# Kernel tuning notes

Hardware: AMD Instinct MI355X
Metric: run time of the kernel (lower is better)

The kernel has to match this reference:

```python
import jax, jax.numpy as jnp
import numpy as np

KD = 128; N_STU_TAB = 20000; N_EXER_TAB = 20000
NS = 4096; NE = 4096; NK = 128
E_SE = 131072; E_EK = 16384; B = 8192
ALPHAS = 0.1; ALPHAE = 0.1; TAU = 0.5


def setup_inputs():
    key = jax.random.key(0)
    ks = jax.random.split(key, 32)
    f = lambda i, shape, s=0.09: jax.random.normal(ks[i], shape, dtype=jnp.float32) * s
    ri = lambda i, shape, hi: jax.random.randint(ks[i], shape, 0, hi)
    inp = {
        'E_stu': f(0, (N_STU_TAB, KD), 0.1),
        'E_exer': f(1, (N_EXER_TAB, KD), 0.1),
        'E_k': f(2, (NK, KD), 0.1),
        'W1': f(3, (KD, KD)), 'a1s': f(4, (KD,)), 'a1d': f(5, (KD,)),
        'W2': f(6, (KD, KD)), 'a2s': f(7, (KD,)), 'a2d': f(8, (KD,)),
        'pW1': f(9, (KD, KD)), 'pW2': f(10, (KD, KD)),
        'pW3': f(11, (KD, KD)), 'pb3': jnp.zeros((KD,), jnp.float32),
        'kn_r': (jax.random.uniform(ks[12], (B, KD)) < 0.25).astype(jnp.float32) + 1e-3,
        'stu_ids': ri(13, (NS,), N_STU_TAB),
        'exer_ids': ri(14, (NE,), N_EXER_TAB),
        'k_ids': jnp.arange(NK),
    }
    j = 15
    for g in ('g0', 'g1', 'g2'):
        inp['se_src_' + g] = ri(j, (E_SE,), NS); j += 1
        inp['se_dst_' + g] = ri(j, (E_SE,), NE); j += 1
        inp['ek_src_' + g] = ri(j, (E_EK,), NE); j += 1
        inp['ek_dst_' + g] = ri(j, (E_EK,), NK); j += 1
    inp['stu_index'] = ri(j, (B,), NS); j += 1
    inp['exer_index'] = ri(j, (B,), NE)
    return inp


def _seg_softmax_agg(scores, msgs, dst, n):
    # numerically-stable softmax over edges grouped by destination node
    m = jax.ops.segment_max(scores, dst, num_segments=n)
    m = jnp.where(jnp.isfinite(m), m, 0.0)
    ex = jnp.exp(scores - m[dst])
    den = jax.ops.segment_sum(ex, dst, num_segments=n)
    alpha = ex / (den[dst] + 1e-16)
    return jax.ops.segment_sum(alpha[:, None] * msgs, dst, num_segments=n)


def _gat(emb, edges, W, a_s, a_d):
    # single-head GAT over hetero edges: stu<->exer, exer<->k
    hs, he, hk = emb['stu'] @ W, emb['exer'] @ W, emb['k'] @ W
    ss_s, ss_e, ss_k = hs @ a_s, he @ a_s, hk @ a_s   # src attention terms
    sd_s, sd_e, sd_k = hs @ a_d, he @ a_d, hk @ a_d   # dst attention terms
    se_src, se_dst, ek_src, ek_dst = edges
    lrelu = lambda x: jax.nn.leaky_relu(x, 0.2)
    # stu <- exer (reverse of stu->exer edges)
    sc = lrelu(ss_e[se_dst] + sd_s[se_src])
    new_s = jax.nn.elu(_seg_softmax_agg(sc, he[se_dst], se_src, NS))
    # exer <- stu  and  exer <- k (softmax spans both relations)
    sc1 = lrelu(ss_s[se_src] + sd_e[se_dst])
    sc2 = lrelu(ss_k[ek_dst] + sd_e[ek_src])
    sc = jnp.concatenate([sc1, sc2])
    msg = jnp.concatenate([hs[se_src], hk[ek_dst]])
    dst = jnp.concatenate([se_dst, ek_src])
    new_e = jax.nn.elu(_seg_softmax_agg(sc, msg, dst, NE))
    # k <- exer
    sc = lrelu(ss_e[ek_src] + sd_k[ek_dst])
    new_k = jax.nn.elu(_seg_softmax_agg(sc, he[ek_src], ek_dst, NK))
    return {'stu': new_s, 'exer': new_e, 'k': new_k}


def _closs(h1, h2):
    z1 = h1 / (jnp.linalg.norm(h1, axis=1, keepdims=True) + 1e-12)
    z2 = h2 / (jnp.linalg.norm(h2, axis=1, keepdims=True) + 1e-12)
    sim = z1 @ z2.T                      # [N, N] cosine similarity
    ex = jnp.exp(sim / TAU)
    pos = jnp.diagonal(ex)
    neg = ex.sum(axis=1) - pos           # off-diagonal sum
    return jnp.mean(-jnp.log(pos / (pos + neg)))


def reference(E_stu, E_exer, E_k, W1, a1s, a1d, W2, a2s, a2d,
              pW1, pW2, pW3, pb3, kn_r,
              stu_ids, exer_ids, k_ids,
              se_src_g0, se_dst_g0, ek_src_g0, ek_dst_g0,
              se_src_g1, se_dst_g1, ek_src_g1, ek_dst_g1,
              se_src_g2, se_dst_g2, ek_src_g2, ek_dst_g2,
              stu_index, exer_index):
    e0 = {'stu': E_stu[stu_ids], 'exer': E_exer[exer_ids], 'k': E_k[k_ids]}

    def run(edges):
        e1 = _gat(e0, edges, W1, a1s, a1d)
        return _gat(e1, edges, W2, a2s, a2d)

    main = run((se_src_g0, se_dst_g0, ek_src_g0, ek_dst_g0))
    v1 = run((se_src_g1, se_dst_g1, ek_src_g1, ek_dst_g1))
    v2 = run((se_src_g2, se_dst_g2, ek_src_g2, ek_dst_g2))

    closs = (ALPHAS * (_closs(v1['stu'], v2['stu']) + _closs(v2['stu'], v1['stu']))
             + ALPHAE * (_closs(v1['exer'], v2['exer']) + _closs(v2['exer'], v1['exer'])))

    bs = main['stu'][stu_index]          # [B, KD]
    be = main['exer'][exer_index]        # [B, KD]
    pref = jax.nn.sigmoid(bs @ pW1.T)
    diff = jax.nn.sigmoid(be @ pW2.T)
    o = jax.nn.sigmoid((pref - diff) @ pW3.T + pb3)
    out = (o * kn_r).sum(axis=1) / kn_r.sum(axis=1)
    return out[:, None], closs
```

## Files before the change

kernel.cpp:

```cpp
#include <hip/hip_runtime.h>
#include <hip/hip_bf16.h>
#include <math.h>

#define KD 128
#define NS 4096
#define NE 4096
#define NK 128
#define NNODE (NS + NE + NK)
#define ESE 131072
#define EEK 16384
#define NCSR (2*ESE + 2*EEK)
#define BQ 8192
#define RP (NNODE + 1)
#define HB 32

typedef __attribute__((ext_vector_type(8))) short short8;
typedef __attribute__((ext_vector_type(4))) short short4_;
typedef __attribute__((ext_vector_type(4))) float float4_;

__device__ __forceinline__ float lrelu_(float x){ return x >= 0.f ? x : 0.2f*x; }
__device__ __forceinline__ float elu_(float x){ return x > 0.f ? x : __expf(x) - 1.f; }
__device__ __forceinline__ float sigm_(float x){ return 1.f/(1.f + __expf(-x)); }
__device__ __forceinline__ float bf2f_(unsigned short u){
  union { unsigned int i; float f; } v; v.i = ((unsigned int)u) << 16; return v.f;
}
__device__ __forceinline__ unsigned short f2b_(float x){
  __hip_bfloat16 b = __float2bfloat16(x); return *(unsigned short*)&b;
}

struct EdgePtrs { const int* s_src[3]; const int* s_dst[3]; const int* e_src[3]; const int* e_dst[3]; };

__global__ __launch_bounds__(256)
void k_fuse1(EdgePtrs ep, int* __restrict__ part,
             const float* __restrict__ W1, const float* __restrict__ a1s,
             const float* __restrict__ a1d,
             unsigned short* __restrict__ hb0, float* __restrict__ ss0,
             float* __restrict__ sd0,
             const float* __restrict__ E_stu, const float* __restrict__ E_exer,
             const float* __restrict__ E_k, const int* __restrict__ sid,
             const int* __restrict__ eid, const int* __restrict__ kid,
             const float* __restrict__ pW1, const float* __restrict__ pW2,
             const float* __restrict__ pW3, unsigned short* __restrict__ pWb,
             const float* __restrict__ W2, unsigned short* __restrict__ w2b) {
  __shared__ __align__(16) char smem[NNODE*4];
  int bid = blockIdx.x, t = threadIdx.x;

  if (bid < 3*HB) {
    int* hcnt = (int*)smem;
    int g = bid / HB, b = bid % HB;
    for (int i = t; i < NNODE; i += 256) hcnt[i] = 0;
    __syncthreads();
    const int* ss_ = ep.s_src[g]; const int* sd_ = ep.s_dst[g];
    const int* es_ = ep.e_src[g]; const int* ed_ = ep.e_dst[g];
    int se0 = b*(ESE/HB);
    for (int i = se0 + t; i < se0 + ESE/HB; i += 256) {
      atomicAdd(&hcnt[ss_[i]], 1);
      atomicAdd(&hcnt[NS + sd_[i]], 1);
    }
    int ek0 = b*(EEK/HB);
    for (int i = ek0 + t; i < ek0 + EEK/HB; i += 256) {
      atomicAdd(&hcnt[NS + es_[i]], 1);
      atomicAdd(&hcnt[NS + NE + ed_[i]], 1);
    }
    __syncthreads();
    int* pp = part + ((size_t)g*HB + b)*NNODE;
    for (int i = t; i < NNODE; i += 256) pp[i] = hcnt[i];
    return;
  }

  if (bid < 3*HB + NNODE/32) {
    float (*ers)[KD] = (float(*)[KD])smem;
    int row0 = (bid - 3*HB)*32;
    int w = t >> 6, c = t & 63;
    for (int i = t; i < 32*KD; i += 256) {
      int r = i >> 7, k = i & 127;
      int gr = row0 + r;
      const float* srow;
      if (gr < NS)           srow = E_stu  + (size_t)sid[gr]*KD;
      else if (gr < NS + NE) srow = E_exer + (size_t)eid[gr - NS]*KD;
      else                   srow = E_k    + (size_t)kid[gr - NS - NE]*KD;
      ers[r][k] = srow[k];
    }
    __syncthreads();
    float acc0[8] = {0,0,0,0,0,0,0,0}, acc1[8] = {0,0,0,0,0,0,0,0};
    #pragma unroll 2
    for (int kc = 0; kc < KD; kc += 4) {
      float wa[4], wb[4];
      #pragma unroll
      for (int j = 0; j < 4; j++) {
        wa[j] = W1[(kc + j)*KD + c];
        wb[j] = W1[(kc + j)*KD + c + 64];
      }
      #pragma unroll
      for (int r = 0; r < 8; r++) {
        float4 e = *(const float4*)&ers[w*8 + r][kc];
        acc0[r] += e.x*wa[0] + e.y*wa[1] + e.z*wa[2] + e.w*wa[3];
        acc1[r] += e.x*wb[0] + e.y*wb[1] + e.z*wb[2] + e.w*wb[3];
      }
    }
    float as1 = a1s[c], as2 = a1s[c + 64], ad1 = a1d[c], ad2 = a1d[c + 64];
    #pragma unroll
    for (int r = 0; r < 8; r++) {
      int gr = row0 + w*8 + r;
      hb0[(size_t)gr*KD + c]      = f2b_(acc0[r]);
      hb0[(size_t)gr*KD + c + 64] = f2b_(acc1[r]);
      float s = acc0[r]*as1 + acc1[r]*as2;
      float d = acc0[r]*ad1 + acc1[r]*ad2;
      #pragma unroll
      for (int off = 32; off; off >>= 1) { s += __shfl_xor(s, off); d += __shfl_xor(d, off); }
      if (c == 0) { ss0[gr] = s; sd0[gr] = d; }
    }
    return;
  }

  {
    int idx = bid - 3*HB - NNODE/32;
    if (idx < 16) {
      float (*tile)[33] = (float(*)[33])smem;
      int tx = t & 31, ty = t >> 5;
      int bx = (idx & 3)*32, by = (idx >> 2)*32;
      for (int j = 0; j < 32; j += 8)
        tile[ty + j][tx] = W2[(by + ty + j)*KD + bx + tx];
      __syncthreads();
      for (int j = 0; j < 32; j += 8)
        w2b[(bx + ty + j)*KD + by + tx] = f2b_(tile[tx][ty + j]);
    } else {
      int r = idx - 16;
      const float* src = r < 4 ? pW1 : (r < 8 ? pW2 : pW3);
      unsigned short* dst = pWb + (size_t)(r >> 2)*KD*KD;
      int off = (r & 3)*4096;
      for (int i = t; i < 1024; i += 256) {
        float4 v = *(const float4*)&src[off + i*4];
        short4_ s;
        s[0] = (short)f2b_(v.x); s[1] = (short)f2b_(v.y);
        s[2] = (short)f2b_(v.z); s[3] = (short)f2b_(v.w);
        *(short4_*)&dst[off + i*4] = s;
      }
    }
  }
}

__global__ void k_sumpart(const int* __restrict__ part, int* __restrict__ cnt_all) {
  int idx = blockIdx.x*256 + threadIdx.x;
  if (idx >= 3*NNODE) return;
  int g = idx / NNODE, n = idx - g*NNODE;
  const int* pg = part + (size_t)g*HB*NNODE + n;
  int s = 0;
  #pragma unroll
  for (int b = 0; b < HB; b++) s += pg[(size_t)b*NNODE];
  cnt_all[idx] = s;
}

__global__ void k_scan(const int* __restrict__ cnt_all, int* __restrict__ rp_all) {
  __shared__ int sums[1024];
  const int CH = (NNODE + 1023) / 1024;
  int g = blockIdx.x, t = threadIdx.x;
  const int* cnt = cnt_all + g*NNODE;
  int* row_ptr = rp_all + g*RP;
  int base = t*CH;
  int local[CH];
  int s = 0;
  for (int j = 0; j < CH; j++) {
    int v = (base + j < NNODE) ? cnt[base + j] : 0;
    local[j] = s; s += v;
  }
  sums[t] = s; __syncthreads();
  for (int off = 1; off < 1024; off <<= 1) {
    int v = (t >= off) ? sums[t - off] : 0;
    __syncthreads();
    sums[t] += v;
    __syncthreads();
  }
  int excl = (t == 0) ? 0 : sums[t - 1];
  for (int j = 0; j < CH; j++)
    if (base + j < NNODE) row_ptr[base + j] = excl + local[j];
  if (t == 1023) row_ptr[NNODE] = sums[1023];
}

__global__ void k_boff(const int* __restrict__ part, const int* __restrict__ rp_all,
                       int* __restrict__ boff) {
  int idx = blockIdx.x*256 + threadIdx.x;
  if (idx >= 3*NNODE) return;
  int g = idx / NNODE, n = idx - g*NNODE;
  const int* pg = part + (size_t)g*HB*NNODE + n;
  int* bg = boff + (size_t)g*HB*NNODE + n;
  int acc = rp_all[g*RP + n];
  #pragma unroll
  for (int b = 0; b < HB; b++) {
    bg[(size_t)b*NNODE] = acc;
    acc += pg[(size_t)b*NNODE];
  }
}

__global__ __launch_bounds__(256)
void k_scatter(EdgePtrs ep, const int* __restrict__ boff, unsigned short* __restrict__ col_all) {
  __shared__ int cur[NNODE];
  int g = blockIdx.y, b = blockIdx.x, t = threadIdx.x;
  const int* bg = boff + ((size_t)g*HB + b)*NNODE;
  for (int i = t; i < NNODE; i += 256) cur[i] = bg[i];
  __syncthreads();
  const int* ss_ = ep.s_src[g]; const int* sd_ = ep.s_dst[g];
  const int* es_ = ep.e_src[g]; const int* ed_ = ep.e_dst[g];
  unsigned short* col = col_all + (size_t)g*NCSR;
  int se0 = b*(ESE/HB);
  for (int i = se0 + t; i < se0 + ESE/HB; i += 256) {
    int s = ss_[i], d = NS + sd_[i];
    col[atomicAdd(&cur[s], 1)] = (unsigned short)d;
    col[atomicAdd(&cur[d], 1)] = (unsigned short)s;
  }
  int ek0 = b*(EEK/HB);
  for (int i = ek0 + t; i < ek0 + EEK/HB; i += 256) {
    int s = NS + es_[i], d = NS + NE + ed_[i];
    col[atomicAdd(&cur[s], 1)] = (unsigned short)d;
    col[atomicAdd(&cur[d], 1)] = (unsigned short)s;
  }
}

__global__ __launch_bounds__(256)
void k_mgemm(const unsigned short* __restrict__ X, const unsigned short* __restrict__ WT,
             const float* __restrict__ a_s, const float* __restrict__ a_d,
             unsigned short* __restrict__ hb, float* __restrict__ ss,
             float* __restrict__ sd) {
  __shared__ unsigned short As[128*KD];
  __shared__ unsigned short Bs[128*KD];
  __shared__ float ssp[128][2], sdp[128][2];
  int t = threadIdx.x;
  const unsigned short* Arow = X + (size_t)blockIdx.x*128*KD;
  #pragma unroll
  for (int j = 0; j < 8; j++) {
    int G = t + j*256;
    int r = G >> 4, g = G & 15;
    int sw = g ^ (r & 15);
    *(float4*)&As[(r*16 + sw)*8] = *(const float4*)&Arow[(size_t)G*8];
    *(float4*)&Bs[(r*16 + sw)*8] = *(const float4*)&WT[(size_t)G*8];
  }
  __syncthreads();
  int w = t >> 6, lane = t & 63;
  int rw = (w >> 1)*64, cw = (w & 1)*64;
  int m15 = lane & 15, quad = lane >> 4;
  float4_ acc[4][4] = {};
  #pragma unroll
  for (int kq = 0; kq < 4; kq++) {
    short8 a[4], b[4];
    int g = kq*4 + quad;
    #pragma unroll
    for (int mi = 0; mi < 4; mi++) {
      int r = rw + mi*16 + m15;
      a[mi] = *(const short8*)&As[(r*16 + (g ^ (r & 15)))*8];
    }
    #pragma unroll
    for (int ni = 0; ni < 4; ni++) {
      int r = cw + ni*16 + m15;
      b[ni] = *(const short8*)&Bs[(r*16 + (g ^ (r & 15)))*8];
    }
    #pragma unroll
    for (int mi = 0; mi < 4; mi++)
      #pragma unroll
      for (int ni = 0; ni < 4; ni++)
        acc[mi][ni] = __builtin_amdgcn_mfma_f32_16x16x32_bf16(a[mi], b[ni], acc[mi][ni], 0, 0, 0);
  }
  int row0 = blockIdx.x*128;
  float asv[4], adv[4];
  #pragma unroll
  for (int ni = 0; ni < 4; ni++) {
    int gc = cw + ni*16 + m15;
    asv[ni] = a_s[gc]; adv[ni] = a_d[gc];
  }
  #pragma unroll
  for (int mi = 0; mi < 4; mi++) {
    #pragma unroll
    for (int reg = 0; reg < 4; reg++) {
      int lr = rw + mi*16 + quad*4 + reg;
      int gr = row0 + lr;
      float s = 0.f, d = 0.f;
      #pragma unroll
      for (int ni = 0; ni < 4; ni++) {
        float v = acc[mi][ni][reg];
        hb[(size_t)gr*KD + cw + ni*16 + m15] = f2b_(v);
        s += v*asv[ni]; d += v*adv[ni];
      }
      s += __shfl_xor(s, 1); d += __shfl_xor(d, 1);
      s += __shfl_xor(s, 2); d += __shfl_xor(d, 2);
      s += __shfl_xor(s, 4); d += __shfl_xor(d, 4);
      s += __shfl_xor(s, 8); d += __shfl_xor(d, 8);
      if (m15 == 0) { ssp[lr][w & 1] = s; sdp[lr][w & 1] = d; }
    }
  }
  __syncthreads();
  if (t < 128) {
    ss[row0 + t] = ssp[t][0] + ssp[t][1];
    sd[row0 + t] = sdp[t][0] + sdp[t][1];
  }
}

__global__ __launch_bounds__(256)
void k_headm(const unsigned short* __restrict__ pWb,
             const float* __restrict__ pb, const float* __restrict__ knr,
             float* __restrict__ out, const float* __restrict__ pbuf,
             const float* __restrict__ g1,
             const int* __restrict__ i1, const int* __restrict__ i2) {
  __shared__ unsigned short At[32*KD];
  __shared__ unsigned short Bt[32*KD];
  __shared__ unsigned short Xt[32*KD];
  __shared__ float nump[32][2], denp[32][2];
  int t = threadIdx.x;
  int row0 = blockIdx.x*32;
  for (int i = t; i < 512; i += 256) {
    int r = i >> 4, g = i & 15;
    int sw = g ^ (r & 15);
    {
      const float* src = &g1[(size_t)i1[row0 + r]*KD + g*8];
      float4 v0 = *(const float4*)src, v1 = *(const float4*)(src + 4);
      short8 s;
      s[0] = (short)f2b_(v0.x); s[1] = (short)f2b_(v0.y);
      s[2] = (short)f2b_(v0.z); s[3] = (short)f2b_(v0.w);
      s[4] = (short)f2b_(v1.x); s[5] = (short)f2b_(v1.y);
      s[6] = (short)f2b_(v1.z); s[7] = (short)f2b_(v1.w);
      *(short8*)&At[(r*16 + sw)*8] = s;
    }
    {
      const float* src = &g1[(size_t)(NS + i2[row0 + r])*KD + g*8];
      float4 v0 = *(const float4*)src, v1 = *(const float4*)(src + 4);
      short8 s;
      s[0] = (short)f2b_(v0.x); s[1] = (short)f2b_(v0.y);
      s[2] = (short)f2b_(v0.z); s[3] = (short)f2b_(v0.w);
      s[4] = (short)f2b_(v1.x); s[5] = (short)f2b_(v1.y);
      s[6] = (short)f2b_(v1.z); s[7] = (short)f2b_(v1.w);
      *(short8*)&Bt[(r*16 + sw)*8] = s;
    }
  }
  __syncthreads();
  int w = t >> 6, lane = t & 63;
  int rw = (w >> 1)*16, cw = (w & 1)*64;
  int m15 = lane & 15, quad = lane >> 4;
  const unsigned short* W1g = pWb;
  const unsigned short* W2g = pWb + KD*KD;
  const unsigned short* W3g = pWb + 2*KD*KD;
  float4_ accP[4] = {}, accD[4] = {};
  #pragma unroll
  for (int kq = 0; kq < 4; kq++) {
    int g = kq*4 + quad;
    int ra = rw + m15;
    short8 a1 = *(const short8*)&At[(ra*16 + (g ^ (ra & 15)))*8];
    short8 a2 = *(const short8*)&Bt[(ra*16 + (g ^ (ra & 15)))*8];
    #pragma unroll
    for (int ni = 0; ni < 4; ni++) {
      int rb = cw + ni*16 + m15;
      short8 b1 = *(const short8*)&W1g[(size_t)rb*KD + g*8];
      short8 b2 = *(const short8*)&W2g[(size_t)rb*KD + g*8];
      accP[ni] = __builtin_amdgcn_mfma_f32_16x16x32_bf16(a1, b1, accP[ni], 0, 0, 0);
      accD[ni] = __builtin_amdgcn_mfma_f32_16x16x32_bf16(a2, b2, accD[ni], 0, 0, 0);
    }
  }
  #pragma unroll
  for (int ni = 0; ni < 4; ni++) {
    #pragma unroll
    for (int reg = 0; reg < 4; reg++) {
      int lr = rw + quad*4 + reg;
      int col = cw + ni*16 + m15;
      float diff = sigm_(accP[ni][reg]) - sigm_(accD[ni][reg]);
      int g2 = col >> 3;
      Xt[(lr*16 + (g2 ^ (lr & 15)))*8 + (col & 7)] = f2b_(diff);
    }
  }
  __syncthreads();
  float4_ accO[4] = {};
  #pragma unroll
  for (int kq = 0; kq < 4; kq++) {
    int g = kq*4 + quad;
    int ra = rw + m15;
    short8 a = *(const short8*)&Xt[(ra*16 + (g ^ (ra & 15)))*8];
    #pragma unroll
    for (int ni = 0; ni < 4; ni++) {
      int rb = cw + ni*16 + m15;
      short8 b = *(const short8*)&W3g[(size_t)rb*KD + g*8];
      accO[ni] = __builtin_amdgcn_mfma_f32_16x16x32_bf16(a, b, accO[ni], 0, 0, 0);
    }
  }
  float pbv[4];
  #pragma unroll
  for (int ni = 0; ni < 4; ni++) pbv[ni] = pb[cw + ni*16 + m15];
  #pragma unroll
  for (int reg = 0; reg < 4; reg++) {
    int lr = rw + quad*4 + reg;
    int gr = row0 + lr;
    float num = 0.f, den = 0.f;
    #pragma unroll
    for (int ni = 0; ni < 4; ni++) {
      float kr = knr[(size_t)gr*KD + cw + ni*16 + m15];
      float o = sigm_(accO[ni][reg] + pbv[ni]);
      num += o*kr; den += kr;
    }
    num += __shfl_xor(num, 1); den += __shfl_xor(den, 1);
    num += __shfl_xor(num, 2); den += __shfl_xor(den, 2);
    num += __shfl_xor(num, 4); den += __shfl_xor(den, 4);
    num += __shfl_xor(num, 8); den += __shfl_xor(den, 8);
    if (m15 == 0) { nump[lr][w & 1] = num; denp[lr][w & 1] = den; }
  }
  __syncthreads();
  if (t < 32)
    out[row0 + t] = (nump[t][0] + nump[t][1]) / (denp[t][0] + denp[t][1]);
  if (blockIdx.x == 0 && w == 0) {
    float v = (lane < 32) ? pbuf[lane] : 0.f;
    #pragma unroll
    for (int off = 32; off; off >>= 1) v += __shfl_xor(v, off);
    if (lane == 0) out[BQ] = 0.1f*v/(float)NS;
  }
}

__global__ __launch_bounds__(256)
void k_agg(const int* __restrict__ rp_all, const unsigned short* __restrict__ col_all,
           const unsigned short* __restrict__ hb_base, const float* __restrict__ ss,
           const float* __restrict__ sd, unsigned short* __restrict__ outb,
           float* __restrict__ out, unsigned short* __restrict__ Zo, int gsel) {
  int wv = blockIdx.x*4 + (threadIdx.x >> 6);
  int lane = threadIdx.x & 63;
  if (wv >= 3*NNODE) return;
  int g = wv / NNODE, node = wv - g*NNODE;
  bool layer2 = (gsel == -2);
  if (layer2 && node >= NS + NE) return;
  const int* rp = rp_all + g*RP;
  const unsigned short* cl = col_all + (size_t)g*NCSR;
  const unsigned short* hgb = layer2 ? hb_base + (size_t)g*NNODE*KD : hb_base;
  const float* ssg = layer2 ? ss + g*NNODE : ss;
  const float* sdg = layer2 ? sd + g*NNODE : sd;
  int e0 = rp[node], e1 = rp[node + 1];
  float sdv = sdg[node];
  int sub = lane >> 4;
  int fl  = lane & 15;
  float l = 0.f;
  float A[8] = {0,0,0,0,0,0,0,0};
  #pragma unroll 4
  for (int e = e0 + sub; e < e1; e += 4) {
    int o = cl[e];
    float pj = __expf(lrelu_(ssg[o] + sdv));
    l += pj;
    short8 mv = *(const short8*)&hgb[(size_t)o*KD + fl*8];
    #pragma unroll
    for (int q = 0; q < 8; q++)
      A[q] += pj * bf2f_((unsigned short)mv[q]);
  }
  l += __shfl_xor(l, 16); l += __shfl_xor(l, 32);
  #pragma unroll
  for (int q = 0; q < 8; q++) {
    A[q] += __shfl_xor(A[q], 16);
    A[q] += __shfl_xor(A[q], 32);
  }
  float inv = 1.f/(l + 1e-16f);
  float av[8];
  #pragma unroll
  for (int q = 0; q < 8; q++) av[q] = elu_(A[q]*inv);
  if (!layer2) {
    if (sub == 0) {
      short8 sv;
      #pragma unroll
      for (int q = 0; q < 8; q++) sv[q] = (short)f2b_(av[q]);
      *(short8*)&outb[(size_t)wv*KD + fl*8] = sv;
    }
    return;
  }
  if (g == 0) {
    if (sub == 0) {
      float* orow = &out[(size_t)node*KD + fl*8];
      *(float4*)orow       = make_float4(av[0], av[1], av[2], av[3]);
      *(float4*)(orow + 4) = make_float4(av[4], av[5], av[6], av[7]);
    }
  } else {
    float nrm = av[0]*av[0] + av[1]*av[1] + av[2]*av[2] + av[3]*av[3]
              + av[4]*av[4] + av[5]*av[5] + av[6]*av[6] + av[7]*av[7];
    #pragma unroll
    for (int off = 1; off <= 8; off <<= 1) nrm += __shfl_xor(nrm, off);
    float invn = 1.f/(sqrtf(nrm) + 1e-12f);
    if (sub == 0) {
      short8 sv;
      #pragma unroll
      for (int q = 0; q < 8; q++) sv[q] = (short)f2b_(av[q]*invn);
      *(short8*)&Zo[((size_t)(g - 1)*8192 + node)*KD + fl*8] = sv;
    }
  }
}

__global__ __launch_bounds__(256)
void k_sim(const unsigned short* __restrict__ Z, float* __restrict__ rsp,
           float* __restrict__ csp, float* __restrict__ dg_all) {
  __shared__ unsigned short As[128*KD];
  __shared__ unsigned short Bs[128*KD];
  int z = blockIdx.z;
  int t = threadIdx.x;
  const unsigned short* Arow = Z + ((size_t)z*NS + (size_t)blockIdx.x*128)*KD;
  const unsigned short* Brow = Z + ((size_t)8192 + (size_t)z*NS + (size_t)blockIdx.y*128)*KD;
  #pragma unroll
  for (int j = 0; j < 8; j++) {
    int G = t + j*256;
    int r = G >> 4, g = G & 15;
    int sw = g ^ (r & 15);
    *(float4*)&As[(r*16 + sw)*8] = *(const float4*)&Arow[(size_t)G*8];
    *(float4*)&Bs[(r*16 + sw)*8] = *(const float4*)&Brow[(size_t)G*8];
  }
  __syncthreads();
  int w = t >> 6, lane = t & 63;
  int rw = (w >> 1)*64, cw = (w & 1)*64;
  int m15 = lane & 15, quad = lane >> 4;
  float4_ acc[4][4] = {};
  #pragma unroll
  for (int kq = 0; kq < 4; kq++) {
    short8 a[4], b[4];
    int g = kq*4 + quad;
    #pragma unroll
    for (int mi = 0; mi < 4; mi++) {
      int r = rw + mi*16 + m15;
      a[mi] = *(const short8*)&As[(r*16 + (g ^ (r & 15)))*8];
    }
    #pragma unroll
    for (int ni = 0; ni < 4; ni++) {
      int r = cw + ni*16 + m15;
      b[ni] = *(const short8*)&Bs[(r*16 + (g ^ (r & 15)))*8];
    }
    #pragma unroll
    for (int mi = 0; mi < 4; mi++)
      #pragma unroll
      for (int ni = 0; ni < 4; ni++)
        acc[mi][ni] = __builtin_amdgcn_mfma_f32_16x16x32_bf16(a[mi], b[ni], acc[mi][ni], 0, 0, 0);
  }
  int i0 = blockIdx.x*128, j0 = blockIdx.y*128;
  float* diag = dg_all + z*NS;
  float* rrow = rsp + ((size_t)z*64 + blockIdx.y*2 + (w & 1))*NS;
  float* crow = csp + ((size_t)z*64 + blockIdx.x*2 + (w >> 1))*NS;
  float cs[4] = {0,0,0,0};
  #pragma unroll
  for (int mi = 0; mi < 4; mi++) {
    float rs[4] = {0,0,0,0};
    #pragma unroll
    for (int ni = 0; ni < 4; ni++) {
      #pragma unroll
      for (int reg = 0; reg < 4; reg++) {
        float sim2 = acc[mi][ni][reg]*2.0f;
        int gi = i0 + rw + mi*16 + quad*4 + reg;
        int gj = j0 + cw + ni*16 + m15;
        if (gi == gj) diag[gi] = sim2;
        float e = __expf(sim2);
        rs[reg] += e; cs[ni] += e;
      }
    }
    #pragma unroll
    for (int reg = 0; reg < 4; reg++) {
      float v = rs[reg];
      v += __shfl_xor(v, 1); v += __shfl_xor(v, 2);
      v += __shfl_xor(v, 4); v += __shfl_xor(v, 8);
      if (m15 == 0) rrow[i0 + rw + mi*16 + quad*4 + reg] = v;
    }
  }
  #pragma unroll
  for (int ni = 0; ni < 4; ni++) {
    float v = cs[ni];
    v += __shfl_xor(v, 16); v += __shfl_xor(v, 32);
    if (quad == 0) crow[j0 + cw + ni*16 + m15] = v;
  }
}

__global__ void k_lred(const float* __restrict__ rsp, const float* __restrict__ csp,
                       const float* __restrict__ dg_all, float* __restrict__ pbuf) {
  __shared__ float red[256];
  int z = blockIdx.y;
  int i = blockIdx.x*256 + threadIdx.x;
  float rs = 0.f, cs = 0.f;
  for (int s = 0; s < 64; s++) {
    rs += rsp[((size_t)z*64 + s)*NS + i];
    cs += csp[((size_t)z*64 + s)*NS + i];
  }
  float v = logf(rs) + logf(cs) - 2.f*dg_all[z*NS + i];
  red[threadIdx.x] = v; __syncthreads();
  for (int off = 128; off; off >>= 1) {
    if (threadIdx.x < off) red[threadIdx.x] += red[threadIdx.x + off];
    __syncthreads();
  }
  if (threadIdx.x == 0) pbuf[z*16 + blockIdx.x] = red[0];
}

extern "C" void kernel_launch(void* const* d_in, const int* in_sizes, int n_in,
                              void* d_out, int out_size, void* d_ws, size_t ws_size,
                              hipStream_t stream) {
  const float* E_stu  = (const float*)d_in[0];
  const float* E_exer = (const float*)d_in[1];
  const float* E_k    = (const float*)d_in[2];
  const float* W1  = (const float*)d_in[3];
  const float* a1s = (const float*)d_in[4];
  const float* a1d = (const float*)d_in[5];
  const float* W2  = (const float*)d_in[6];
  const float* a2s = (const float*)d_in[7];
  const float* a2d = (const float*)d_in[8];
  const float* pW1 = (const float*)d_in[9];
  const float* pW2 = (const float*)d_in[10];
  const float* pW3 = (const float*)d_in[11];
  const float* pb3 = (const float*)d_in[12];
  const float* kn_r = (const float*)d_in[13];
  const int* stu_ids  = (const int*)d_in[14];
  const int* exer_ids = (const int*)d_in[15];
  const int* k_ids    = (const int*)d_in[16];
  EdgePtrs ep;
  for (int g = 0; g < 3; g++) {
    ep.s_src[g] = (const int*)d_in[17 + g*4];
    ep.s_dst[g] = (const int*)d_in[18 + g*4];
    ep.e_src[g] = (const int*)d_in[19 + g*4];
    ep.e_dst[g] = (const int*)d_in[20 + g*4];
  }
  const int* stu_index  = (const int*)d_in[29];
  const int* exer_index = (const int*)d_in[30];
  float* out = (float*)d_out;

  char* p = (char*)d_ws;
  auto carve = [&](size_t bytes) -> char* {
    char* r = p; p += (bytes + 255) & ~(size_t)255; return r;
  };
  const size_t NODE_F = (size_t)NNODE*KD;
  float* ssb = (float*)carve((size_t)8*NNODE*4);
  float* ss0 = ssb,            *sd0 = ssb + NNODE;
  float* ss3 = ssb + 2*NNODE,  *sd3 = ssb + 5*NNODE;
  unsigned short* hb0 = (unsigned short*)carve(NODE_F*2);
  unsigned short* hb3 = (unsigned short*)carve(3*NODE_F*2);
  char* Creg = carve((size_t)8*HB*NNODE*4);
  int*   part = (int*)Creg;
  int*   boff = (int*)Creg + (size_t)3*HB*NNODE;
  unsigned short* etb = (unsigned short*)Creg;
  float* eoutAll = (float*)carve((size_t)(NS + NE)*KD*4);
  int* cnt_all = (int*)carve((size_t)3*NNODE*4);
  int* rp_all  = (int*)carve((size_t)3*RP*4);
  unsigned short* col_all = (unsigned short*)carve((size_t)3*NCSR*2);
  unsigned short* pWb = (unsigned short*)carve((size_t)3*KD*KD*2);
  float* rsp = (float*)carve((size_t)2*64*NS*4);
  float* csp = (float*)carve((size_t)2*64*NS*4);
  float* dg_all = (float*)carve((size_t)2*NS*4);
  float* pbuf = (float*)carve(64*4);
  unsigned short* Z = (unsigned short*)carve((size_t)2*8192*KD*2);
  unsigned short* w2b = (unsigned short*)carve((size_t)KD*KD*2);

  k_fuse1<<<3*HB + NNODE/32 + 16 + 12, 256, 0, stream>>>(
      ep, part, W1, a1s, a1d, hb0, ss0, sd0,
      E_stu, E_exer, E_k, stu_ids, exer_ids, k_ids,
      pW1, pW2, pW3, pWb, W2, w2b);

  k_sumpart<<<(3*NNODE + 255)/256, 256, 0, stream>>>(part, cnt_all);
  k_scan<<<3, 1024, 0, stream>>>(cnt_all, rp_all);
  k_boff<<<(3*NNODE + 255)/256, 256, 0, stream>>>(part, rp_all, boff);
  k_scatter<<<dim3(HB, 3), 256, 0, stream>>>(ep, boff, col_all);

  k_agg<<<3*NNODE/4, 256, 0, stream>>>(rp_all, col_all, hb0, ss0, sd0, etb,
                                       nullptr, nullptr, -1);

  k_mgemm<<<3*NNODE/128, 256, 0, stream>>>(etb, w2b, a2s, a2d, hb3, ss3, sd3);
  k_agg<<<3*NNODE/4, 256, 0, stream>>>(rp_all, col_all, hb3, ss3, sd3, nullptr,
                                       eoutAll, Z, -2);

  k_sim<<<dim3(32, 32, 2), 256, 0, stream>>>(Z, rsp, csp, dg_all);
  k_lred<<<dim3(16, 2), 256, 0, stream>>>(rsp, csp, dg_all, pbuf);

  k_headm<<<BQ/32, 256, 0, stream>>>(pWb, pb3, kn_r,
                                     out, pbuf, eoutAll, stu_index, exer_index);
}
```

Measured before the change: 275.2 us.

## Fuse prediction head into similarity kernel and finalize loss via atomics

Merges the prediction-head kernel into the contrastive-similarity kernel as extra blocks of one launch, so the two independent workloads share the GPU and one launch is removed. The main-view aggregation output is now stored as bf16 rather than fp32, which halves that write and lets the head load it without converting. The final loss reduction moves into k_lred through an atomic accumulator and a last-block counter, with the accumulator reset in k_boff. In exchange it adds atomics and a threadfence-based completion pattern, and the fused kernel's shared-memory footprint is sized for the similarity path.

New measurement: 270.1 us. About the same (-1.8%).

```diff
diff --git a/kernel.cpp b/kernel.cpp
--- a/kernel.cpp
+++ b/kernel.cpp
@@ -178,8 +178,9 @@
 }
 
 __global__ void k_boff(const int* __restrict__ part, const int* __restrict__ rp_all,
-                       int* __restrict__ boff) {
+                       int* __restrict__ boff, float* __restrict__ clbuf) {
   int idx = blockIdx.x*256 + threadIdx.x;
+  if (idx == 0) { clbuf[0] = 0.f; ((int*)clbuf)[1] = 0; }
   if (idx >= 3*NNODE) return;
   int g = idx / NNODE, n = idx - g*NNODE;
   const int* pg = part + (size_t)g*HB*NNODE + n;
@@ -294,125 +295,10 @@
 }
 
 __global__ __launch_bounds__(256)
-void k_headm(const unsigned short* __restrict__ pWb,
-             const float* __restrict__ pb, const float* __restrict__ knr,
-             float* __restrict__ out, const float* __restrict__ pbuf,
-             const float* __restrict__ g1,
-             const int* __restrict__ i1, const int* __restrict__ i2) {
-  __shared__ unsigned short At[32*KD];
-  __shared__ unsigned short Bt[32*KD];
-  __shared__ unsigned short Xt[32*KD];
-  __shared__ float nump[32][2], denp[32][2];
-  int t = threadIdx.x;
-  int row0 = blockIdx.x*32;
-  for (int i = t; i < 512; i += 256) {
-    int r = i >> 4, g = i & 15;
-    int sw = g ^ (r & 15);
-    {
-      const float* src = &g1[(size_t)i1[row0 + r]*KD + g*8];
-      float4 v0 = *(const float4*)src, v1 = *(const float4*)(src + 4);
-      short8 s;
-      s[0] = (short)f2b_(v0.x); s[1] = (short)f2b_(v0.y);
-      s[2] = (short)f2b_(v0.z); s[3] = (short)f2b_(v0.w);
-      s[4] = (short)f2b_(v1.x); s[5] = (short)f2b_(v1.y);
-      s[6] = (short)f2b_(v1.z); s[7] = (short)f2b_(v1.w);
-      *(short8*)&At[(r*16 + sw)*8] = s;
-    }
-    {
-      const float* src = &g1[(size_t)(NS + i2[row0 + r])*KD + g*8];
-      float4 v0 = *(const float4*)src, v1 = *(const float4*)(src + 4);
-      short8 s;
-      s[0] = (short)f2b_(v0.x); s[1] = (short)f2b_(v0.y);
-      s[2] = (short)f2b_(v0.z); s[3] = (short)f2b_(v0.w);
-      s[4] = (short)f2b_(v1.x); s[5] = (short)f2b_(v1.y);
-      s[6] = (short)f2b_(v1.z); s[7] = (short)f2b_(v1.w);
-      *(short8*)&Bt[(r*16 + sw)*8] = s;
-    }
-  }
-  __syncthreads();
-  int w = t >> 6, lane = t & 63;
-  int rw = (w >> 1)*16, cw = (w & 1)*64;
-  int m15 = lane & 15, quad = lane >> 4;
-  const unsigned short* W1g = pWb;
-  const unsigned short* W2g = pWb + KD*KD;
-  const unsigned short* W3g = pWb + 2*KD*KD;
-  float4_ accP[4] = {}, accD[4] = {};
-  #pragma unroll
-  for (int kq = 0; kq < 4; kq++) {
-    int g = kq*4 + quad;
-    int ra = rw + m15;
-    short8 a1 = *(const short8*)&At[(ra*16 + (g ^ (ra & 15)))*8];
-    short8 a2 = *(const short8*)&Bt[(ra*16 + (g ^ (ra & 15)))*8];
-    #pragma unroll
-    for (int ni = 0; ni < 4; ni++) {
-      int rb = cw + ni*16 + m15;
-      short8 b1 = *(const short8*)&W1g[(size_t)rb*KD + g*8];
-      short8 b2 = *(const short8*)&W2g[(size_t)rb*KD + g*8];
-      accP[ni] = __builtin_amdgcn_mfma_f32_16x16x32_bf16(a1, b1, accP[ni], 0, 0, 0);
-      accD[ni] = __builtin_amdgcn_mfma_f32_16x16x32_bf16(a2, b2, accD[ni], 0, 0, 0);
-    }
-  }
-  #pragma unroll
-  for (int ni = 0; ni < 4; ni++) {
-    #pragma unroll
-    for (int reg = 0; reg < 4; reg++) {
-      int lr = rw + quad*4 + reg;
-      int col = cw + ni*16 + m15;
-      float diff = sigm_(accP[ni][reg]) - sigm_(accD[ni][reg]);
-      int g2 = col >> 3;
-      Xt[(lr*16 + (g2 ^ (lr & 15)))*8 + (col & 7)] = f2b_(diff);
-    }
-  }
-  __syncthreads();
-  float4_ accO[4] = {};
-  #pragma unroll
-  for (int kq = 0; kq < 4; kq++) {
-    int g = kq*4 + quad;
-    int ra = rw + m15;
-    short8 a = *(const short8*)&Xt[(ra*16 + (g ^ (ra & 15)))*8];
-    #pragma unroll
-    for (int ni = 0; ni < 4; ni++) {
-      int rb = cw + ni*16 + m15;
-      short8 b = *(const short8*)&W3g[(size_t)rb*KD + g*8];
-      accO[ni] = __builtin_amdgcn_mfma_f32_16x16x32_bf16(a, b, accO[ni], 0, 0, 0);
-    }
-  }
-  float pbv[4];
-  #pragma unroll
-  for (int ni = 0; ni < 4; ni++) pbv[ni] = pb[cw + ni*16 + m15];
-  #pragma unroll
-  for (int reg = 0; reg < 4; reg++) {
-    int lr = rw + quad*4 + reg;
-    int gr = row0 + lr;
-    float num = 0.f, den = 0.f;
-    #pragma unroll
-    for (int ni = 0; ni < 4; ni++) {
-      float kr = knr[(size_t)gr*KD + cw + ni*16 + m15];
-      float o = sigm_(accO[ni][reg] + pbv[ni]);
-      num += o*kr; den += kr;
-    }
-    num += __shfl_xor(num, 1); den += __shfl_xor(den, 1);
-    num += __shfl_xor(num, 2); den += __shfl_xor(den, 2);
-    num += __shfl_xor(num, 4); den += __shfl_xor(den, 4);
-    num += __shfl_xor(num, 8); den += __shfl_xor(den, 8);
-    if (m15 == 0) { nump[lr][w & 1] = num; denp[lr][w & 1] = den; }
-  }
-  __syncthreads();
-  if (t < 32)
-    out[row0 + t] = (nump[t][0] + nump[t][1]) / (denp[t][0] + denp[t][1]);
-  if (blockIdx.x == 0 && w == 0) {
-    float v = (lane < 32) ? pbuf[lane] : 0.f;
-    #pragma unroll
-    for (int off = 32; off; off >>= 1) v += __shfl_xor(v, off);
-    if (lane == 0) out[BQ] = 0.1f*v/(float)NS;
-  }
-}
-
-__global__ __launch_bounds__(256)
 void k_agg(const int* __restrict__ rp_all, const unsigned short* __restrict__ col_all,
            const unsigned short* __restrict__ hb_base, const float* __restrict__ ss,
            const float* __restrict__ sd, unsigned short* __restrict__ outb,
-           float* __restrict__ out, unsigned short* __restrict__ Zo, int gsel) {
+           unsigned short* __restrict__ eoutb, unsigned short* __restrict__ Zo, int gsel) {
   int wv = blockIdx.x*4 + (threadIdx.x >> 6);
   int lane = threadIdx.x & 63;
   if (wv >= 3*NNODE) return;
@@ -461,9 +347,10 @@
   }
   if (g == 0) {
     if (sub == 0) {
-      float* orow = &out[(size_t)node*KD + fl*8];
-      *(float4*)orow       = make_float4(av[0], av[1], av[2], av[3]);
-      *(float4*)(orow + 4) = make_float4(av[4], av[5], av[6], av[7]);
+      short8 sv;
+      #pragma unroll
+      for (int q = 0; q < 8; q++) sv[q] = (short)f2b_(av[q]);
+      *(short8*)&eoutb[(size_t)node*KD + fl*8] = sv;
     }
   } else {
     float nrm = av[0]*av[0] + av[1]*av[1] + av[2]*av[2] + av[3]*av[3]
@@ -481,85 +368,184 @@
 }
 
 __global__ __launch_bounds__(256)
-void k_sim(const unsigned short* __restrict__ Z, float* __restrict__ rsp,
-           float* __restrict__ csp, float* __restrict__ dg_all) {
-  __shared__ unsigned short As[128*KD];
-  __shared__ unsigned short Bs[128*KD];
-  int z = blockIdx.z;
-  int t = threadIdx.x;
-  const unsigned short* Arow = Z + ((size_t)z*NS + (size_t)blockIdx.x*128)*KD;
-  const unsigned short* Brow = Z + ((size_t)8192 + (size_t)z*NS + (size_t)blockIdx.y*128)*KD;
-  #pragma unroll
-  for (int j = 0; j < 8; j++) {
-    int G = t + j*256;
-    int r = G >> 4, g = G & 15;
-    int sw = g ^ (r & 15);
-    *(float4*)&As[(r*16 + sw)*8] = *(const float4*)&Arow[(size_t)G*8];
-    *(float4*)&Bs[(r*16 + sw)*8] = *(const float4*)&Brow[(size_t)G*8];
-  }
-  __syncthreads();
-  int w = t >> 6, lane = t & 63;
-  int rw = (w >> 1)*64, cw = (w & 1)*64;
-  int m15 = lane & 15, quad = lane >> 4;
-  float4_ acc[4][4] = {};
-  #pragma unroll
-  for (int kq = 0; kq < 4; kq++) {
-    short8 a[4], b[4];
-    int g = kq*4 + quad;
+void k_simhead(const unsigned short* __restrict__ Z, float* __restrict__ rsp,
+               float* __restrict__ csp, float* __restrict__ dg_all,
+               const unsigned short* __restrict__ pWb,
+               const float* __restrict__ pb, const float* __restrict__ knr,
+               float* __restrict__ out, const unsigned short* __restrict__ eoutb,
+               const int* __restrict__ i1, const int* __restrict__ i2) {
+  __shared__ __align__(16) unsigned short U[2*128*KD];
+  int bid = blockIdx.x, t = threadIdx.x;
+
+  if (bid < BQ/32) {
+    unsigned short* At = U;
+    unsigned short* Bt = U + 32*KD;
+    unsigned short* Xt = U + 64*KD;
+    float (*nump)[2] = (float(*)[2])(U + 96*KD);
+    float (*denp)[2] = (float(*)[2])(U + 96*KD + 128);
+    int row0 = bid*32;
+    for (int i = t; i < 512; i += 256) {
+      int r = i >> 4, g = i & 15;
+      int sw = g ^ (r & 15);
+      *(short8*)&At[(r*16 + sw)*8] =
+          *(const short8*)&eoutb[(size_t)i1[row0 + r]*KD + g*8];
+      *(short8*)&Bt[(r*16 + sw)*8] =
+          *(const short8*)&eoutb[(size_t)(NS + i2[row0 + r])*KD + g*8];
+    }
+    __syncthreads();
+    int w = t >> 6, lane = t & 63;
+    int rw = (w >> 1)*16, cw = (w & 1)*64;
+    int m15 = lane & 15, quad = lane >> 4;
+    const unsigned short* W1g = pWb;
+    const unsigned short* W2g = pWb + KD*KD;
+    const unsigned short* W3g = pWb + 2*KD*KD;
+    float4_ accP[4] = {}, accD[4] = {};
+    #pragma unroll
+    for (int kq = 0; kq < 4; kq++) {
+      int g = kq*4 + quad;
+      int ra = rw + m15;
+      short8 a1 = *(const short8*)&At[(ra*16 + (g ^ (ra & 15)))*8];
+      short8 a2 = *(const short8*)&Bt[(ra*16 + (g ^ (ra & 15)))*8];
+      #pragma unroll
+      for (int ni = 0; ni < 4; ni++) {
+        int rb = cw + ni*16 + m15;
+        short8 b1 = *(const short8*)&W1g[(size_t)rb*KD + g*8];
+        short8 b2 = *(const short8*)&W2g[(size_t)rb*KD + g*8];
+        accP[ni] = __builtin_amdgcn_mfma_f32_16x16x32_bf16(a1, b1, accP[ni], 0, 0, 0);
+        accD[ni] = __builtin_amdgcn_mfma_f32_16x16x32_bf16(a2, b2, accD[ni], 0, 0, 0);
+      }
+    }
+    #pragma unroll
+    for (int ni = 0; ni < 4; ni++) {
+      #pragma unroll
+      for (int reg = 0; reg < 4; reg++) {
+        int lr = rw + quad*4 + reg;
+        int col = cw + ni*16 + m15;
+        float diff = sigm_(accP[ni][reg]) - sigm_(accD[ni][reg]);
+        int g2 = col >> 3;
+        Xt[(lr*16 + (g2 ^ (lr & 15)))*8 + (col & 7)] = f2b_(diff);
+      }
+    }
+    __syncthreads();
+    float4_ accO[4] = {};
+    #pragma unroll
+    for (int kq = 0; kq < 4; kq++) {
+      int g = kq*4 + quad;
+      int ra = rw + m15;
+      short8 a = *(const short8*)&Xt[(ra*16 + (g ^ (ra & 15)))*8];
+      #pragma unroll
+      for (int ni = 0; ni < 4; ni++) {
+        int rb = cw + ni*16 + m15;
+        short8 b = *(const short8*)&W3g[(size_t)rb*KD + g*8];
+        accO[ni] = __builtin_amdgcn_mfma_f32_16x16x32_bf16(a, b, accO[ni], 0, 0, 0);
+      }
+    }
+    float pbv[4];
+    #pragma unroll
+    for (int ni = 0; ni < 4; ni++) pbv[ni] = pb[cw + ni*16 + m15];
+    #pragma unroll
+    for (int reg = 0; reg < 4; reg++) {
+      int lr = rw + quad*4 + reg;
+      int gr = row0 + lr;
+      float num = 0.f, den = 0.f;
+      #pragma unroll
+      for (int ni = 0; ni < 4; ni++) {
+        float kr = knr[(size_t)gr*KD + cw + ni*16 + m15];
+        float o = sigm_(accO[ni][reg] + pbv[ni]);
+        num += o*kr; den += kr;
+      }
+      num += __shfl_xor(num, 1); den += __shfl_xor(den, 1);
+      num += __shfl_xor(num, 2); den += __shfl_xor(den, 2);
+      num += __shfl_xor(num, 4); den += __shfl_xor(den, 4);
+      num += __shfl_xor(num, 8); den += __shfl_xor(den, 8);
+      if (m15 == 0) { nump[lr][w & 1] = num; denp[lr][w & 1] = den; }
+    }
+    __syncthreads();
+    if (t < 32)
+      out[row0 + t] = (nump[t][0] + nump[t][1]) / (denp[t][0] + denp[t][1]);
+    return;
+  }
+
+  {
+    unsigned short* As = U;
+    unsigned short* Bs = U + 128*KD;
+    int sb = bid - BQ/32;
+    int bx = sb & 31, by = (sb >> 5) & 31, z = sb >> 10;
+    const unsigned short* Arow = Z + ((size_t)z*NS + (size_t)bx*128)*KD;
+    const unsigned short* Brow = Z + ((size_t)8192 + (size_t)z*NS + (size_t)by*128)*KD;
+    #pragma unroll
+    for (int j = 0; j < 8; j++) {
+      int G = t + j*256;
+      int r = G >> 4, g = G & 15;
+      int sw = g ^ (r & 15);
+      *(float4*)&As[(r*16 + sw)*8] = *(const float4*)&Arow[(size_t)G*8];
+      *(float4*)&Bs[(r*16 + sw)*8] = *(const float4*)&Brow[(size_t)G*8];
+    }
+    __syncthreads();
+    int w = t >> 6, lane = t & 63;
+    int rw = (w >> 1)*64, cw = (w & 1)*64;
+    int m15 = lane & 15, quad = lane >> 4;
+    float4_ acc[4][4] = {};
+    #pragma unroll
+    for (int kq = 0; kq < 4; kq++) {
+      short8 a[4], b[4];
+      int g = kq*4 + quad;
+      #pragma unroll
+      for (int mi = 0; mi < 4; mi++) {
+        int r = rw + mi*16 + m15;
+        a[mi] = *(const short8*)&As[(r*16 + (g ^ (r & 15)))*8];
+      }
+      #pragma unroll
+      for (int ni = 0; ni < 4; ni++) {
+        int r = cw + ni*16 + m15;
+        b[ni] = *(const short8*)&Bs[(r*16 + (g ^ (r & 15)))*8];
+      }
+      #pragma unroll
+      for (int mi = 0; mi < 4; mi++)
+        #pragma unroll
+        for (int ni = 0; ni < 4; ni++)
+          acc[mi][ni] = __builtin_amdgcn_mfma_f32_16x16x32_bf16(a[mi], b[ni], acc[mi][ni], 0, 0, 0);
+    }
+    int i0 = bx*128, j0 = by*128;
+    float* diag = dg_all + z*NS;
+    float* rrow = rsp + ((size_t)z*64 + by*2 + (w & 1))*NS;
+    float* crow = csp + ((size_t)z*64 + bx*2 + (w >> 1))*NS;
+    float cs[4] = {0,0,0,0};
     #pragma unroll
     for (int mi = 0; mi < 4; mi++) {
-      int r = rw + mi*16 + m15;
-      a[mi] = *(const short8*)&As[(r*16 + (g ^ (r & 15)))*8];
+      float rs[4] = {0,0,0,0};
+      #pragma unroll
+      for (int ni = 0; ni < 4; ni++) {
+        #pragma unroll
+        for (int reg = 0; reg < 4; reg++) {
+          float sim2 = acc[mi][ni][reg]*2.0f;
+          int gi = i0 + rw + mi*16 + quad*4 + reg;
+          int gj = j0 + cw + ni*16 + m15;
+          if (gi == gj) diag[gi] = sim2;
+          float e = __expf(sim2);
+          rs[reg] += e; cs[ni] += e;
+        }
+      }
+      #pragma unroll
+      for (int reg = 0; reg < 4; reg++) {
+        float v = rs[reg];
+        v += __shfl_xor(v, 1); v += __shfl_xor(v, 2);
+        v += __shfl_xor(v, 4); v += __shfl_xor(v, 8);
+        if (m15 == 0) rrow[i0 + rw + mi*16 + quad*4 + reg] = v;
+      }
     }
     #pragma unroll
     for (int ni = 0; ni < 4; ni++) {
-      int r = cw + ni*16 + m15;
-      b[ni] = *(const short8*)&Bs[(r*16 + (g ^ (r & 15)))*8];
-    }
-    #pragma unroll
-    for (int mi = 0; mi < 4; mi++)
-      #pragma unroll
-      for (int ni = 0; ni < 4; ni++)
-        acc[mi][ni] = __builtin_amdgcn_mfma_f32_16x16x32_bf16(a[mi], b[ni], acc[mi][ni], 0, 0, 0);
-  }
-  int i0 = blockIdx.x*128, j0 = blockIdx.y*128;
-  float* diag = dg_all + z*NS;
-  float* rrow = rsp + ((size_t)z*64 + blockIdx.y*2 + (w & 1))*NS;
-  float* crow = csp + ((size_t)z*64 + blockIdx.x*2 + (w >> 1))*NS;
-  float cs[4] = {0,0,0,0};
-  #pragma unroll
-  for (int mi = 0; mi < 4; mi++) {
-    float rs[4] = {0,0,0,0};
-    #pragma unroll
-    for (int ni = 0; ni < 4; ni++) {
-      #pragma unroll
-      for (int reg = 0; reg < 4; reg++) {
-        float sim2 = acc[mi][ni][reg]*2.0f;
-        int gi = i0 + rw + mi*16 + quad*4 + reg;
-        int gj = j0 + cw + ni*16 + m15;
-        if (gi == gj) diag[gi] = sim2;
-        float e = __expf(sim2);
-        rs[reg] += e; cs[ni] += e;
-      }
-    }
-    #pragma unroll
-    for (int reg = 0; reg < 4; reg++) {
-      float v = rs[reg];
-      v += __shfl_xor(v, 1); v += __shfl_xor(v, 2);
-      v += __shfl_xor(v, 4); v += __shfl_xor(v, 8);
-      if (m15 == 0) rrow[i0 + rw + mi*16 + quad*4 + reg] = v;
-    }
-  }
-  #pragma unroll
-  for (int ni = 0; ni < 4; ni++) {
-    float v = cs[ni];
-    v += __shfl_xor(v, 16); v += __shfl_xor(v, 32);
-    if (quad == 0) crow[j0 + cw + ni*16 + m15] = v;
+      float v = cs[ni];
+      v += __shfl_xor(v, 16); v += __shfl_xor(v, 32);
+      if (quad == 0) crow[j0 + cw + ni*16 + m15] = v;
+    }
   }
 }
 
 __global__ void k_lred(const float* __restrict__ rsp, const float* __restrict__ csp,
-                       const float* __restrict__ dg_all, float* __restrict__ pbuf) {
+                       const float* __restrict__ dg_all, float* __restrict__ out,
+                       float* __restrict__ clbuf) {
   __shared__ float red[256];
   int z = blockIdx.y;
   int i = blockIdx.x*256 + threadIdx.x;
@@ -574,7 +560,16 @@
     if (threadIdx.x < off) red[threadIdx.x] += red[threadIdx.x + off];
     __syncthreads();
   }
-  if (threadIdx.x == 0) pbuf[z*16 + blockIdx.x] = red[0];
+  if (threadIdx.x == 0) {
+    atomicAdd(&clbuf[0], red[0]);
+    __threadfence();
+    int old = atomicAdd((int*)&clbuf[1], 1);
+    if (old == 31) {
+      __threadfence();
+      float tot = atomicAdd(&clbuf[0], 0.0f);
+      out[BQ] = 0.1f*tot/(float)NS;
+    }
+  }
 }
 
 extern "C" void kernel_launch(void* const* d_in, const int* in_sizes, int n_in,
@@ -622,7 +617,7 @@
   int*   part = (int*)Creg;
   int*   boff = (int*)Creg + (size_t)3*HB*NNODE;
   unsigned short* etb = (unsigned short*)Creg;
-  float* eoutAll = (float*)carve((size_t)(NS + NE)*KD*4);
+  unsigned short* eoutb = (unsigned short*)carve((size_t)(NS + NE)*KD*2);
   int* cnt_all = (int*)carve((size_t)3*NNODE*4);
   int* rp_all  = (int*)carve((size_t)3*RP*4);
   unsigned short* col_all = (unsigned short*)carve((size_t)3*NCSR*2);
@@ -630,7 +625,7 @@
   float* rsp = (float*)carve((size_t)2*64*NS*4);
   float* csp = (float*)carve((size_t)2*64*NS*4);
   float* dg_all = (float*)carve((size_t)2*NS*4);
-  float* pbuf = (float*)carve(64*4);
+  float* clbuf = (float*)carve(256);
   unsigned short* Z = (unsigned short*)carve((size_t)2*8192*KD*2);
   unsigned short* w2b = (unsigned short*)carve((size_t)KD*KD*2);
 
@@ -641,7 +636,7 @@
 
   k_sumpart<<<(3*NNODE + 255)/256, 256, 0, stream>>>(part, cnt_all);
   k_scan<<<3, 1024, 0, stream>>>(cnt_all, rp_all);
-  k_boff<<<(3*NNODE + 255)/256, 256, 0, stream>>>(part, rp_all, boff);
+  k_boff<<<(3*NNODE + 255)/256, 256, 0, stream>>>(part, rp_all, boff, clbuf);
   k_scatter<<<dim3(HB, 3), 256, 0, stream>>>(ep, boff, col_all);
 
   k_agg<<<3*NNODE/4, 256, 0, stream>>>(rp_all, col_all, hb0, ss0, sd0, etb,
@@ -649,11 +644,11 @@
 
   k_mgemm<<<3*NNODE/128, 256, 0, stream>>>(etb, w2b, a2s, a2d, hb3, ss3, sd3);
   k_agg<<<3*NNODE/4, 256, 0, stream>>>(rp_all, col_all, hb3, ss3, sd3, nullptr,
-                                       eoutAll, Z, -2);
-
-  k_sim<<<dim3(32, 32, 2), 256, 0, stream>>>(Z, rsp, csp, dg_all);
-  k_lred<<<dim3(16, 2), 256, 0, stream>>>(rsp, csp, dg_all, pbuf);
-
-  k_headm<<<BQ/32, 256, 0, stream>>>(pWb, pb3, kn_r,
-                                     out, pbuf, eoutAll, stu_index, exer_index);
-}
+                                       eoutb, Z, -2);
+
+  k_simhead<<<BQ/32 + 2048, 256, 0, stream>>>(Z, rsp, csp, dg_all,
+                                              pWb, pb3, kn_r, out, eoutb,
+                                              stu_index, exer_index);
+
+  k_lred<<<dim3(16, 2), 256, 0, stream>>>(rsp, csp, dg_all, out, clbuf);
+}
```
